# Performance work log

Measured on AMD Instinct MI355X. Metric: run time of the kernel, lower is better.

The kernel has to match this reference:

```python
import math
import jax, jax.numpy as jnp
import numpy as np

H = 16  # n_heads


def setup_inputs() -> dict:
    key = jax.random.key(0)
    ks = jax.random.split(key, 12)
    b, n, dm = 4, 1024, 1024
    s = 1.0 / math.sqrt(dm)
    inp = {
        'query': jax.random.normal(ks[0], (b, n, dm), jnp.float32),
        'key':   jax.random.normal(ks[1], (b, n, dm), jnp.float32),
        'value': jax.random.normal(ks[2], (b, n, dm), jnp.float32),
        'Wq': jax.random.normal(ks[3], (dm, dm), jnp.float32) * s,
        'bq': jnp.zeros((dm,), jnp.float32),
        'Wk': jax.random.normal(ks[4], (dm, dm), jnp.float32) * s,
        'bk': jnp.zeros((dm,), jnp.float32),
        'Wv': jax.random.normal(ks[5], (dm, dm), jnp.float32) * s,
        'bv': jnp.zeros((dm,), jnp.float32),
        'Wo': jax.random.normal(ks[6], (dm, dm), jnp.float32) * s,
        'bo': jnp.zeros((dm,), jnp.float32),
    }
    return inp


def reference(query, key, value, Wq, bq, Wk, bk, Wv, bv, Wo, bo):
    b, n, dm = query.shape
    dk = dm // H

    def proj(x, W, bias):
        # Linear(d_model,d_model) then split heads: [b,n,dm] -> [b,h,n,dk]
        y = x @ W.T + bias
        return y.reshape(b, n, H, dk).transpose(0, 2, 1, 3)

    q = proj(query, Wq, bq)
    k = proj(key, Wk, bk)
    v = proj(value, Wv, bv)

    scores = jnp.einsum('bhid,bhjd->bhij', q, k) / math.sqrt(dk)  # [b,h,n,n]
    p_attn = jax.nn.softmax(scores, axis=-1)
    # softmax(ones) along last dim is exactly uniform 1/n
    p_ident = jnp.full_like(scores, 1.0 / n)
    rnd = jax.random.normal(jax.random.key(42), scores.shape, scores.dtype)
    p_rand = jax.nn.softmax(rnd, axis=-1)

    # FAITHFUL to source: einsum('b h i j, b h i d -> b h i d', p, value)
    # i.e. value scaled by row-sum of the attention probs (== value up to numerics)
    def weight(p):
        return v * jnp.sum(p, axis=-1, keepdims=True)  # [b,h,n,dk]

    x = weight(p_attn)
    y = weight(p_ident)
    z = weight(p_rand)

    def merge(t):  # [b,h,n,dk] -> [b,n,dm]
        return t.transpose(0, 2, 1, 3).reshape(b, n, dm)

    return (merge(x) @ Wo.T + bo, merge(y), merge(z))
```

## Files before the change

### kernel.cpp

```cpp
#include <hip/hip_runtime.h>
#include <hip/hip_bf16.h>
#include <stdint.h>

using bf16 = __hip_bfloat16;
typedef __attribute__((ext_vector_type(8))) __bf16 bf16x8;
typedef __attribute__((ext_vector_type(4))) float f32x4;

static __device__ __forceinline__ bf16 f2b(float x) { return __float2bfloat16(x); }
static __device__ __forceinline__ uint32_t pack2(float a, float b) {
    bf16 ha = f2b(a), hb = f2b(b);
    return (uint32_t)(*(const uint16_t*)&ha) | ((uint32_t)(*(const uint16_t*)&hb) << 16);
}

__global__ __launch_bounds__(256) void prep_kernel(
    const float* __restrict__ value, const float* __restrict__ Wv,
    const float* __restrict__ Wo, const float* __restrict__ bv,
    const float* __restrict__ bo,
    bf16* __restrict__ value_b, bf16* __restrict__ Wv_b,
    bf16* __restrict__ Wo_b, bf16* __restrict__ WvT_b, float* __restrict__ bc,
    int nbVal, int nbWv, int nbWo, int nbT, int dm)
{
    __shared__ bf16 tile[32][34];
    const int b = blockIdx.x;
    const int tid = threadIdx.x;

    if (b < nbVal) {
        const size_t i = ((size_t)b * 256 + tid) * 8;
        const float4 v0 = *(const float4*)(value + i);
        const float4 v1 = *(const float4*)(value + i + 4);
        uint4 u = { pack2(v0.x, v0.y), pack2(v0.z, v0.w),
                    pack2(v1.x, v1.y), pack2(v1.z, v1.w) };
        *(uint4*)(value_b + i) = u;
    } else if (b < nbVal + nbWv) {
        const size_t i = ((size_t)(b - nbVal) * 256 + tid) * 8;
        const float4 v0 = *(const float4*)(Wv + i);
        const float4 v1 = *(const float4*)(Wv + i + 4);
        uint4 u = { pack2(v0.x, v0.y), pack2(v0.z, v0.w),
                    pack2(v1.x, v1.y), pack2(v1.z, v1.w) };
        *(uint4*)(Wv_b + i) = u;
    } else if (b < nbVal + nbWv + nbWo) {
        const size_t i = ((size_t)(b - nbVal - nbWv) * 256 + tid) * 8;
        const float4 v0 = *(const float4*)(Wo + i);
        const float4 v1 = *(const float4*)(Wo + i + 4);
        uint4 u = { pack2(v0.x, v0.y), pack2(v0.z, v0.w),
                    pack2(v1.x, v1.y), pack2(v1.z, v1.w) };
        *(uint4*)(Wo_b + i) = u;
    } else if (b < nbVal + nbWv + nbWo + nbT) {
        const int t = b - nbVal - nbWv - nbWo;
        const int tpr = dm / 32;
        const int i0 = (t / tpr) * 32, j0 = (t % tpr) * 32;
        const int tx = tid & 31, ty = tid >> 5;
        #pragma unroll
        for (int p = 0; p < 4; ++p) {
            const int r = ty + p * 8;
            tile[r][tx] = f2b(Wv[(size_t)(i0 + r) * dm + j0 + tx]);
        }
        __syncthreads();
        #pragma unroll
        for (int p = 0; p < 4; ++p) {
            const int c = ty + p * 8;
            WvT_b[(size_t)(j0 + c) * dm + i0 + tx] = tile[tx][c];
        }
    } else {
        const int lane = tid & 63;
        const int wave = tid >> 6;
        const int row = (b - nbVal - nbWv - nbWo - nbT) * 4 + wave;
        const float* wrow = Wo + (size_t)row * dm;
        float s = 0.f;
        for (int k = lane * 4; k < dm; k += 256) {
            const float4 w = *(const float4*)(wrow + k);
            const float4 x = *(const float4*)(bv + k);
            s += w.x * x.x + w.y * x.y + w.z * x.z + w.w * x.w;
        }
        #pragma unroll
        for (int off = 32; off >= 1; off >>= 1) s += __shfl_down(s, off, 64);
        if (lane == 0) bc[row] = s + bo[row];
    }
}

__global__ __launch_bounds__(256) void wc_gemm(
    const bf16* __restrict__ A, const bf16* __restrict__ B,
    bf16* __restrict__ C, int N, int K)
{
    __shared__ bf16 As[64 * 64];
    __shared__ bf16 Bs[64 * 64];

    const int tid = threadIdx.x;
    const int lane = tid & 63;
    const int wave = tid >> 6;
    const int wm = (wave >> 1) * 32;
    const int wn = (wave & 1) * 32;
    const int bm = blockIdx.x * 64;
    const int bn = blockIdx.y * 64;

    f32x4 acc[2][2] = {};

    const int s0 = wave * 128 + lane;
    const int s1 = s0 + 64;
    const int r0 = s0 >> 3, r1 = s1 >> 3;
    const int p0 = (s0 & 7) ^ (r0 & 7);
    const int p1 = (s1 & 7) ^ (r1 & 7);
    const bf16* gA0 = A + (size_t)(bm + r0) * K + p0 * 8;
    const bf16* gA1 = A + (size_t)(bm + r1) * K + p1 * 8;
    const bf16* gB0 = B + (size_t)(bn + r0) * K + p0 * 8;
    const bf16* gB1 = B + (size_t)(bn + r1) * K + p1 * 8;
    bf16* lA0 = As + s0 * 8;
    bf16* lA1 = As + s1 * 8;
    bf16* lB0 = Bs + s0 * 8;
    bf16* lB1 = Bs + s1 * 8;

    const int fr = lane & 15;
    const int fkc = lane >> 4;

    for (int k0 = 0; k0 < K; k0 += 64) {
        __builtin_amdgcn_global_load_lds(
            (const __attribute__((address_space(1))) void*)(gA0 + k0),
            (__attribute__((address_space(3))) void*)lA0, 16, 0, 0);
        __builtin_amdgcn_global_load_lds(
            (const __attribute__((address_space(1))) void*)(gA1 + k0),
            (__attribute__((address_space(3))) void*)lA1, 16, 0, 0);
        __builtin_amdgcn_global_load_lds(
            (const __attribute__((address_space(1))) void*)(gB0 + k0),
            (__attribute__((address_space(3))) void*)lB0, 16, 0, 0);
        __builtin_amdgcn_global_load_lds(
            (const __attribute__((address_space(1))) void*)(gB1 + k0),
            (__attribute__((address_space(3))) void*)lB1, 16, 0, 0);
        __syncthreads();

        #pragma unroll
        for (int kk = 0; kk < 2; ++kk) {
            const int xsw = ((kk * 4 + fkc) ^ (fr & 7)) * 8;
            bf16x8 af[2], bg[2];
            #pragma unroll
            for (int u = 0; u < 2; ++u) {
                af[u] = *(const bf16x8*)(As + (wm + u * 16 + fr) * 64 + xsw);
                bg[u] = *(const bf16x8*)(Bs + (wn + u * 16 + fr) * 64 + xsw);
            }
            #pragma unroll
            for (int i = 0; i < 2; ++i)
                #pragma unroll
                for (int j = 0; j < 2; ++j)
                    acc[i][j] = __builtin_amdgcn_mfma_f32_16x16x32_bf16(
                        af[i], bg[j], acc[i][j], 0, 0, 0);
        }
        __syncthreads();
    }

    const int quad = lane >> 4;
    #pragma unroll
    for (int j = 0; j < 2; ++j) {
        const int col = bn + wn + j * 16 + fr;
        #pragma unroll
        for (int i = 0; i < 2; ++i) {
            const int row0 = bm + wm + i * 16 + quad * 4;
            #pragma unroll
            for (int r = 0; r < 4; ++r)
                C[(size_t)(row0 + r) * N + col] = f2b(acc[i][j][r]);
        }
    }
}

#define TM 128
#define TN 128
#define BK 32

__global__ __launch_bounds__(256) void gemm_fused(
    const bf16* __restrict__ A, const bf16* __restrict__ Bcat,
    const float* __restrict__ bv, const float* __restrict__ bc,
    float* __restrict__ out0, float* __restrict__ out1, float* __restrict__ out2,
    int M, int dm)
{
    __shared__ bf16 As[TM * BK];
    __shared__ bf16 Bs[TN * BK];
    __shared__ float Es[4][16 * 68];

    const int K = dm;
    const int tid = threadIdx.x;
    const int lane = tid & 63;
    const int wave = tid >> 6;
    const int wm = (wave >> 1) * 64;
    const int wn = (wave & 1) * 64;
    const int bm = blockIdx.x * TM;
    const int bn = blockIdx.y * TN;

    f32x4 acc[4][4] = {};

    const int s0 = wave * 128 + lane;
    const int s1 = s0 + 64;
    const int r0 = s0 >> 2, r1 = s1 >> 2;
    const int p0 = (s0 & 3) ^ (r0 & 3) ^ ((r0 >> 2) & 3);
    const int p1 = (s1 & 3) ^ (r1 & 3) ^ ((r1 >> 2) & 3);
    const bf16* gA0 = A + (size_t)(bm + r0) * K + p0 * 8;
    const bf16* gA1 = A + (size_t)(bm + r1) * K + p1 * 8;
    const bf16* gB0 = Bcat + (size_t)(bn + r0) * K + p0 * 8;
    const bf16* gB1 = Bcat + (size_t)(bn + r1) * K + p1 * 8;
    bf16* lA0 = As + s0 * 8;
    bf16* lA1 = As + s1 * 8;
    bf16* lB0 = Bs + s0 * 8;
    bf16* lB1 = Bs + s1 * 8;

    const int fr = lane & 15;
    const int fkc = lane >> 4;
    const int xsw = fkc ^ (fr & 3) ^ ((fr >> 2) & 3);

    for (int k0 = 0; k0 < K; k0 += BK) {
        __builtin_amdgcn_global_load_lds(
            (const __attribute__((address_space(1))) void*)(gA0 + k0),
            (__attribute__((address_space(3))) void*)lA0, 16, 0, 0);
        __builtin_amdgcn_global_load_lds(
            (const __attribute__((address_space(1))) void*)(gA1 + k0),
            (__attribute__((address_space(3))) void*)lA1, 16, 0, 0);
        __builtin_amdgcn_global_load_lds(
            (const __attribute__((address_space(1))) void*)(gB0 + k0),
            (__attribute__((address_space(3))) void*)lB0, 16, 0, 0);
        __builtin_amdgcn_global_load_lds(
            (const __attribute__((address_space(1))) void*)(gB1 + k0),
            (__attribute__((address_space(3))) void*)lB1, 16, 0, 0);
        __syncthreads();

        bf16x8 af[4], bg[4];
        #pragma unroll
        for (int t = 0; t < 4; ++t) {
            af[t] = *(const bf16x8*)(As + (wm + t * 16 + fr) * BK + xsw * 8);
            bg[t] = *(const bf16x8*)(Bs + (wn + t * 16 + fr) * BK + xsw * 8);
        }
        #pragma unroll
        for (int i = 0; i < 4; ++i)
            #pragma unroll
            for (int j = 0; j < 4; ++j)
                acc[i][j] = __builtin_amdgcn_mfma_f32_16x16x32_bf16(
                    af[i], bg[j], acc[i][j], 0, 0, 0);
        __syncthreads();
    }

    const bool second = (bn >= dm);
    const int colbase = bn + wn - (second ? dm : 0);
    const float* bias = second ? bc : bv;
    float* o0 = second ? out0 : out1;
    float* o1 = second ? nullptr : out2;

    float bb[4];
    #pragma unroll
    for (int j = 0; j < 4; ++j) bb[j] = bias[colbase + j * 16 + fr];

    float* E = &Es[wave][0];
    const int quad = lane >> 4;
    const int cc = (lane & 15) * 4;

    #pragma unroll
    for (int i = 0; i < 4; ++i) {
        #pragma unroll
        for (int j = 0; j < 4; ++j)
            #pragma unroll
            for (int r = 0; r < 4; ++r)
                E[(quad * 4 + r) * 68 + j * 16 + fr] = acc[i][j][r] + bb[j];
        #pragma unroll
        for (int ph = 0; ph < 4; ++ph) {
            const int row = quad * 4 + ph;
            const float4 v = *(const float4*)(E + row * 68 + cc);
            const size_t gi = (size_t)(bm + wm + i * 16 + row) * dm + colbase + cc;
            *(float4*)(o0 + gi) = v;
            if (o1) *(float4*)(o1 + gi) = v;
        }
    }
}

__global__ __launch_bounds__(256) void gemm_f32_naive(
    const float* __restrict__ A, const float* __restrict__ B,
    const float* __restrict__ bias,
    float* __restrict__ C0, float* __restrict__ C1,
    int M, int N, int K)
{
    const size_t idx = (size_t)blockIdx.x * 256 + threadIdx.x;
    if (idx >= (size_t)M * N) return;
    const int row = (int)(idx / N), col = (int)(idx % N);
    const float* a = A + (size_t)row * K;
    const float* b = B + (size_t)col * K;
    float s = bias ? bias[col] : 0.0f;
    for (int k = 0; k < K; ++k) s += a[k] * b[k];
    C0[idx] = s;
    if (C1) C1[idx] = s;
}

extern "C" void kernel_launch(void* const* d_in, const int* in_sizes, int n_in,
                              void* d_out, int out_size, void* d_ws, size_t ws_size,
                              hipStream_t stream)
{
    const float* value = (const float*)d_in[2];
    const float* Wv    = (const float*)d_in[7];
    const float* bv    = (const float*)d_in[8];
    const float* Wo    = (const float*)d_in[9];
    const float* bo    = (const float*)d_in[10];

    const int dm = in_sizes[8];
    const int M  = in_sizes[2] / dm;
    const size_t MN = (size_t)M * dm;

    float* out0 = (float*)d_out;
    float* out1 = out0 + MN;
    float* out2 = out1 + MN;

    const size_t dm2 = (size_t)dm * dm;
    const size_t need = MN * 2 + dm2 * 2 * 4 + (size_t)dm * 4;
    const bool ok = (ws_size >= need) && (M % TM == 0) && (dm % TM == 0) &&
                    (MN % 2048 == 0) && (dm2 % 2048 == 0) &&
                    (dm % 64 == 0) && (dm % 4 == 0);
    if (ok) {
        char* ws = (char*)d_ws;
        bf16* value_b = (bf16*)ws;   ws += MN * 2;
        bf16* Wv_b    = (bf16*)ws;   ws += dm2 * 2;
        bf16* Wc_b    = (bf16*)ws;   ws += dm2 * 2;
        bf16* Wo_b    = (bf16*)ws;   ws += dm2 * 2;
        bf16* WvT_b   = (bf16*)ws;   ws += dm2 * 2;
        float* bc     = (float*)ws;

        const int nbVal = (int)(MN / 2048);
        const int nbWv  = (int)(dm2 / 2048);
        const int nbWo  = nbWv;
        const int nbT   = (dm / 32) * (dm / 32);
        const int nbBc  = dm / 4;
        prep_kernel<<<nbVal + nbWv + nbWo + nbT + nbBc, 256, 0, stream>>>(
            value, Wv, Wo, bv, bo, value_b, Wv_b, Wo_b, WvT_b, bc,
            nbVal, nbWv, nbWo, nbT, dm);

        dim3 gwc(dm / 64, dm / 64);
        wc_gemm<<<gwc, 256, 0, stream>>>(Wo_b, WvT_b, Wc_b, dm, dm);

        dim3 grid(M / TM, 2 * dm / TN);
        gemm_fused<<<grid, 256, 0, stream>>>(value_b, Wv_b, bv, bc,
                                             out0, out1, out2, M, dm);
    } else {
        const int nblk = (int)((MN + 255) / 256);
        gemm_f32_naive<<<nblk, 256, 0, stream>>>(value, Wv, bv, out1, out2, M, dm, dm);
        gemm_f32_naive<<<nblk, 256, 0, stream>>>(out1, Wo, bo, out0, nullptr, M, dm, dm);
    }
}
```

Measured before the change: 160.0 us.

## Overlap value conversion with Wc GEMM and merge Wv cast into transpose pass

Splits preprocessing so the weight-only work (Wo cast, Wv cast and transpose) runs first. The Wc = Wo·Wv GEMM then shares a single launch with the value fp32-to-bf16 conversion and the bias-combine reduction, so the bandwidth-bound conversion can overlap the small GEMM. The Wv cast now writes both the plain and transposed bf16 copies from one read, which removes a redundant pass over Wv. Occupancy hints are added to the mix and fused GEMM kernels, which may constrain register allocation.

Measured after the change: 154.2 us. -3.7%, faster.

```diff
diff --git a/kernel.cpp b/kernel.cpp
--- a/kernel.cpp
+++ b/kernel.cpp
@@ -12,59 +12,141 @@
     return (uint32_t)(*(const uint16_t*)&ha) | ((uint32_t)(*(const uint16_t*)&hb) << 16);
 }
 
-__global__ __launch_bounds__(256) void prep_kernel(
-    const float* __restrict__ value, const float* __restrict__ Wv,
-    const float* __restrict__ Wo, const float* __restrict__ bv,
-    const float* __restrict__ bo,
-    bf16* __restrict__ value_b, bf16* __restrict__ Wv_b,
-    bf16* __restrict__ Wo_b, bf16* __restrict__ WvT_b, float* __restrict__ bc,
-    int nbVal, int nbWv, int nbWo, int nbT, int dm)
+__global__ __launch_bounds__(256) void prep_w_kernel(
+    const float* __restrict__ Wv, const float* __restrict__ Wo,
+    bf16* __restrict__ Wv_b, bf16* __restrict__ Wo_b, bf16* __restrict__ WvT_b,
+    int nbWo, int dm)
 {
     __shared__ bf16 tile[32][34];
     const int b = blockIdx.x;
     const int tid = threadIdx.x;
 
-    if (b < nbVal) {
+    if (b < nbWo) {
         const size_t i = ((size_t)b * 256 + tid) * 8;
+        const float4 v0 = *(const float4*)(Wo + i);
+        const float4 v1 = *(const float4*)(Wo + i + 4);
+        uint4 u = { pack2(v0.x, v0.y), pack2(v0.z, v0.w),
+                    pack2(v1.x, v1.y), pack2(v1.z, v1.w) };
+        *(uint4*)(Wo_b + i) = u;
+    } else {
+        const int t = b - nbWo;
+        const int tpr = dm / 32;
+        const int i0 = (t / tpr) * 32, j0 = (t % tpr) * 32;
+        const int tx = tid & 31, ty = tid >> 5;
+        #pragma unroll
+        for (int p = 0; p < 4; ++p) {
+            const int r = ty + p * 8;
+            const bf16 h = f2b(Wv[(size_t)(i0 + r) * dm + j0 + tx]);
+            Wv_b[(size_t)(i0 + r) * dm + j0 + tx] = h;
+            tile[r][tx] = h;
+        }
+        __syncthreads();
+        #pragma unroll
+        for (int p = 0; p < 4; ++p) {
+            const int c = ty + p * 8;
+            WvT_b[(size_t)(j0 + c) * dm + i0 + tx] = tile[tx][c];
+        }
+    }
+}
+
+__global__ __launch_bounds__(256, 4) void mix_kernel(
+    const bf16* __restrict__ A, const bf16* __restrict__ B,
+    const float* __restrict__ value, const float* __restrict__ Wo,
+    const float* __restrict__ bv, const float* __restrict__ bo,
+    bf16* __restrict__ Wc_b, bf16* __restrict__ value_b, float* __restrict__ bc,
+    int nbWc, int nbVal, int dm)
+{
+    __shared__ bf16 As[64 * 64];
+    __shared__ bf16 Bs[64 * 64];
+
+    const int blk = blockIdx.x;
+    const int tid = threadIdx.x;
+
+    if (blk < nbWc) {
+        const int K = dm, N = dm;
+        const int tpr = dm / 64;
+        const int bm = (blk / tpr) * 64, bn = (blk % tpr) * 64;
+        const int lane = tid & 63;
+        const int wave = tid >> 6;
+        const int wm = (wave >> 1) * 32;
+        const int wn = (wave & 1) * 32;
+
+        f32x4 acc[2][2] = {};
+
+        const int s0 = wave * 128 + lane;
+        const int s1 = s0 + 64;
+        const int r0 = s0 >> 3, r1 = s1 >> 3;
+        const int p0 = (s0 & 7) ^ (r0 & 7);
+        const int p1 = (s1 & 7) ^ (r1 & 7);
+        const bf16* gA0 = A + (size_t)(bm + r0) * K + p0 * 8;
+        const bf16* gA1 = A + (size_t)(bm + r1) * K + p1 * 8;
+        const bf16* gB0 = B + (size_t)(bn + r0) * K + p0 * 8;
+        const bf16* gB1 = B + (size_t)(bn + r1) * K + p1 * 8;
+        bf16* lA0 = As + s0 * 8;
+        bf16* lA1 = As + s1 * 8;
+        bf16* lB0 = Bs + s0 * 8;
+        bf16* lB1 = Bs + s1 * 8;
+
+        const int fr = lane & 15;
+        const int fkc = lane >> 4;
+
+        for (int k0 = 0; k0 < K; k0 += 64) {
+            __builtin_amdgcn_global_load_lds(
+                (const __attribute__((address_space(1))) void*)(gA0 + k0),
+                (__attribute__((address_space(3))) void*)lA0, 16, 0, 0);
+            __builtin_amdgcn_global_load_lds(
+                (const __attribute__((address_space(1))) void*)(gA1 + k0),
+                (__attribute__((address_space(3))) void*)lA1, 16, 0, 0);
+            __builtin_amdgcn_global_load_lds(
+                (const __attribute__((address_space(1))) void*)(gB0 + k0),
+                (__attribute__((address_space(3))) void*)lB0, 16, 0, 0);
+            __builtin_amdgcn_global_load_lds(
+                (const __attribute__((address_space(1))) void*)(gB1 + k0),
+                (__attribute__((address_space(3))) void*)lB1, 16, 0, 0);
+            __syncthreads();
+
+            #pragma unroll
+            for (int kk = 0; kk < 2; ++kk) {
+                const int xsw = ((kk * 4 + fkc) ^ (fr & 7)) * 8;
+                bf16x8 af[2], bg[2];
+                #pragma unroll
+                for (int u = 0; u < 2; ++u) {
+                    af[u] = *(const bf16x8*)(As + (wm + u * 16 + fr) * 64 + xsw);
+                    bg[u] = *(const bf16x8*)(Bs + (wn + u * 16 + fr) * 64 + xsw);
+                }
+                #pragma unroll
+                for (int i = 0; i < 2; ++i)
+                    #pragma unroll
+                    for (int j = 0; j < 2; ++j)
+                        acc[i][j] = __builtin_amdgcn_mfma_f32_16x16x32_bf16(
+                            af[i], bg[j], acc[i][j], 0, 0, 0);
+            }
+            __syncthreads();
+        }
+
+        const int quad = lane >> 4;
+        #pragma unroll
+        for (int j = 0; j < 2; ++j) {
+            const int col = bn + wn + j * 16 + fr;
+            #pragma unroll
+            for (int i = 0; i < 2; ++i) {
+                const int row0 = bm + wm + i * 16 + quad * 4;
+                #pragma unroll
+                for (int r = 0; r < 4; ++r)
+                    Wc_b[(size_t)(row0 + r) * N + col] = f2b(acc[i][j][r]);
+            }
+        }
+    } else if (blk < nbWc + nbVal) {
+        const size_t i = ((size_t)(blk - nbWc) * 256 + tid) * 8;
         const float4 v0 = *(const float4*)(value + i);
         const float4 v1 = *(const float4*)(value + i + 4);
         uint4 u = { pack2(v0.x, v0.y), pack2(v0.z, v0.w),
                     pack2(v1.x, v1.y), pack2(v1.z, v1.w) };
         *(uint4*)(value_b + i) = u;
-    } else if (b < nbVal + nbWv) {
-        const size_t i = ((size_t)(b - nbVal) * 256 + tid) * 8;
-        const float4 v0 = *(const float4*)(Wv + i);
-        const float4 v1 = *(const float4*)(Wv + i + 4);
-        uint4 u = { pack2(v0.x, v0.y), pack2(v0.z, v0.w),
-                    pack2(v1.x, v1.y), pack2(v1.z, v1.w) };
-        *(uint4*)(Wv_b + i) = u;
-    } else if (b < nbVal + nbWv + nbWo) {
-        const size_t i = ((size_t)(b - nbVal - nbWv) * 256 + tid) * 8;
-        const float4 v0 = *(const float4*)(Wo + i);
-        const float4 v1 = *(const float4*)(Wo + i + 4);
-        uint4 u = { pack2(v0.x, v0.y), pack2(v0.z, v0.w),
-                    pack2(v1.x, v1.y), pack2(v1.z, v1.w) };
-        *(uint4*)(Wo_b + i) = u;
-    } else if (b < nbVal + nbWv + nbWo + nbT) {
-        const int t = b - nbVal - nbWv - nbWo;
-        const int tpr = dm / 32;
-        const int i0 = (t / tpr) * 32, j0 = (t % tpr) * 32;
-        const int tx = tid & 31, ty = tid >> 5;
-        #pragma unroll
-        for (int p = 0; p < 4; ++p) {
-            const int r = ty + p * 8;
-            tile[r][tx] = f2b(Wv[(size_t)(i0 + r) * dm + j0 + tx]);
-        }
-        __syncthreads();
-        #pragma unroll
-        for (int p = 0; p < 4; ++p) {
-            const int c = ty + p * 8;
-            WvT_b[(size_t)(j0 + c) * dm + i0 + tx] = tile[tx][c];
-        }
     } else {
         const int lane = tid & 63;
         const int wave = tid >> 6;
-        const int row = (b - nbVal - nbWv - nbWo - nbT) * 4 + wave;
+        const int row = (blk - nbWc - nbVal) * 4 + wave;
         const float* wrow = Wo + (size_t)row * dm;
         float s = 0.f;
         for (int k = lane * 4; k < dm; k += 256) {
@@ -78,93 +160,11 @@
     }
 }
 
-__global__ __launch_bounds__(256) void wc_gemm(
-    const bf16* __restrict__ A, const bf16* __restrict__ B,
-    bf16* __restrict__ C, int N, int K)
-{
-    __shared__ bf16 As[64 * 64];
-    __shared__ bf16 Bs[64 * 64];
-
-    const int tid = threadIdx.x;
-    const int lane = tid & 63;
-    const int wave = tid >> 6;
-    const int wm = (wave >> 1) * 32;
-    const int wn = (wave & 1) * 32;
-    const int bm = blockIdx.x * 64;
-    const int bn = blockIdx.y * 64;
-
-    f32x4 acc[2][2] = {};
-
-    const int s0 = wave * 128 + lane;
-    const int s1 = s0 + 64;
-    const int r0 = s0 >> 3, r1 = s1 >> 3;
-    const int p0 = (s0 & 7) ^ (r0 & 7);
-    const int p1 = (s1 & 7) ^ (r1 & 7);
-    const bf16* gA0 = A + (size_t)(bm + r0) * K + p0 * 8;
-    const bf16* gA1 = A + (size_t)(bm + r1) * K + p1 * 8;
-    const bf16* gB0 = B + (size_t)(bn + r0) * K + p0 * 8;
-    const bf16* gB1 = B + (size_t)(bn + r1) * K + p1 * 8;
-    bf16* lA0 = As + s0 * 8;
-    bf16* lA1 = As + s1 * 8;
-    bf16* lB0 = Bs + s0 * 8;
-    bf16* lB1 = Bs + s1 * 8;
-
-    const int fr = lane & 15;
-    const int fkc = lane >> 4;
-
-    for (int k0 = 0; k0 < K; k0 += 64) {
-        __builtin_amdgcn_global_load_lds(
-            (const __attribute__((address_space(1))) void*)(gA0 + k0),
-            (__attribute__((address_space(3))) void*)lA0, 16, 0, 0);
-        __builtin_amdgcn_global_load_lds(
-            (const __attribute__((address_space(1))) void*)(gA1 + k0),
-            (__attribute__((address_space(3))) void*)lA1, 16, 0, 0);
-        __builtin_amdgcn_global_load_lds(
-            (const __attribute__((address_space(1))) void*)(gB0 + k0),
-            (__attribute__((address_space(3))) void*)lB0, 16, 0, 0);
-        __builtin_amdgcn_global_load_lds(
-            (const __attribute__((address_space(1))) void*)(gB1 + k0),
-            (__attribute__((address_space(3))) void*)lB1, 16, 0, 0);
-        __syncthreads();
-
-        #pragma unroll
-        for (int kk = 0; kk < 2; ++kk) {
-            const int xsw = ((kk * 4 + fkc) ^ (fr & 7)) * 8;
-            bf16x8 af[2], bg[2];
-            #pragma unroll
-            for (int u = 0; u < 2; ++u) {
-                af[u] = *(const bf16x8*)(As + (wm + u * 16 + fr) * 64 + xsw);
-                bg[u] = *(const bf16x8*)(Bs + (wn + u * 16 + fr) * 64 + xsw);
-            }
-            #pragma unroll
-            for (int i = 0; i < 2; ++i)
-                #pragma unroll
-                for (int j = 0; j < 2; ++j)
-                    acc[i][j] = __builtin_amdgcn_mfma_f32_16x16x32_bf16(
-                        af[i], bg[j], acc[i][j], 0, 0, 0);
-        }
-        __syncthreads();
-    }
-
-    const int quad = lane >> 4;
-    #pragma unroll
-    for (int j = 0; j < 2; ++j) {
-        const int col = bn + wn + j * 16 + fr;
-        #pragma unroll
-        for (int i = 0; i < 2; ++i) {
-            const int row0 = bm + wm + i * 16 + quad * 4;
-            #pragma unroll
-            for (int r = 0; r < 4; ++r)
-                C[(size_t)(row0 + r) * N + col] = f2b(acc[i][j][r]);
-        }
-    }
-}
-
 #define TM 128
 #define TN 128
 #define BK 32
 
-__global__ __launch_bounds__(256) void gemm_fused(
+__global__ __launch_bounds__(256, 4) void gemm_fused(
     const bf16* __restrict__ A, const bf16* __restrict__ Bcat,
     const float* __restrict__ bv, const float* __restrict__ bc,
     float* __restrict__ out0, float* __restrict__ out1, float* __restrict__ out2,
@@ -314,17 +314,17 @@
         bf16* WvT_b   = (bf16*)ws;   ws += dm2 * 2;
         float* bc     = (float*)ws;
 
+        const int nbWo  = (int)(dm2 / 2048);
+        const int nbT   = (dm / 32) * (dm / 32);
+        prep_w_kernel<<<nbWo + nbT, 256, 0, stream>>>(
+            Wv, Wo, Wv_b, Wo_b, WvT_b, nbWo, dm);
+
+        const int nbWc  = (dm / 64) * (dm / 64);
         const int nbVal = (int)(MN / 2048);
-        const int nbWv  = (int)(dm2 / 2048);
-        const int nbWo  = nbWv;
-        const int nbT   = (dm / 32) * (dm / 32);
         const int nbBc  = dm / 4;
-        prep_kernel<<<nbVal + nbWv + nbWo + nbT + nbBc, 256, 0, stream>>>(
-            value, Wv, Wo, bv, bo, value_b, Wv_b, Wo_b, WvT_b, bc,
-            nbVal, nbWv, nbWo, nbT, dm);
-
-        dim3 gwc(dm / 64, dm / 64);
-        wc_gemm<<<gwc, 256, 0, stream>>>(Wo_b, WvT_b, Wc_b, dm, dm);
+        mix_kernel<<<nbWc + nbVal + nbBc, 256, 0, stream>>>(
+            Wo_b, WvT_b, value, Wo, bv, bo, Wc_b, value_b, bc,
+            nbWc, nbVal, dm);
 
         dim3 grid(M / TM, 2 * dm / TN);
         gemm_fused<<<grid, 256, 0, stream>>>(value_b, Wv_b, bv, bc,
```
